# Optimization experiments

Measured on AMD Instinct MI355X. Metric: run time of the kernel, lower is better.

Reference implementation:

```python
import jax, jax.numpy as jnp
import numpy as np

B, S, D_MODEL, D_QK, D_VO = 4, 2048, 1024, 128, 128
NEG = -1.0e9


def setup_inputs() -> dict:
    key = jax.random.key(0)
    k1, k2, k3, k4, k5 = jax.random.split(key, 5)
    enc = jax.random.normal(k1, (B, S, D_MODEL), dtype=jnp.float32)
    # causal mask: True means masked (masked_fill), broadcast over batch
    causal = jnp.triu(jnp.ones((S, S), dtype=bool), k=1)
    mask = jnp.broadcast_to(causal, (B, S, S))
    scale = 0.02
    W_q = jax.random.normal(k2, (D_MODEL, D_QK), dtype=jnp.float32) * scale
    W_k = jax.random.normal(k3, (D_MODEL, D_QK), dtype=jnp.float32) * scale
    W_v = jax.random.normal(k4, (D_MODEL, D_VO), dtype=jnp.float32) * scale
    W_o = jax.random.normal(k5, (D_VO, D_MODEL), dtype=jnp.float32) * scale
    return {"encodings": enc, "mask": mask, "W_q": W_q, "W_k": W_k, "W_v": W_v, "W_o": W_o}


def reference(encodings, mask, W_q, W_k, W_v, W_o):
    # q,k: [B,S,d_qk]; v: [B,S,d_vo]
    q = jnp.einsum('bsd,de->bse', encodings, W_q)
    k = jnp.einsum('bsd,de->bse', encodings, W_k)
    v = jnp.einsum('bsd,de->bse', encodings, W_v)
    sims = jnp.einsum('bqe,bke->bqk', q, k) / jnp.asarray(D_QK ** 0.5, q.dtype)
    sims = jnp.where(mask, jnp.asarray(NEG, sims.dtype), sims)
    attn = jax.nn.softmax(sims, axis=-1)  # [B,S,S]
    scores = jnp.einsum('bqk,bke->bqe', attn, v)  # [B,S,d_vo]
    return jnp.einsum('bse,ed->bsd', scores, W_o)  # [B,S,d_model]
```

## Files before the change

### kernel.cpp

```cpp
#include <hip/hip_runtime.h>
#include <hip/hip_bf16.h>
#include <stdint.h>

typedef __attribute__((ext_vector_type(8))) short short8;
typedef __attribute__((ext_vector_type(4))) float floatx4;

using bf16 = __hip_bfloat16;

#define SCALE_L2 0.12751793359133147f

__device__ inline unsigned short f2b(float f) {
    bf16 h = __float2bfloat16(f);
    return *(unsigned short*)&h;
}
__device__ inline float b2f(unsigned short u) {
    union { unsigned int i; float f; } v;
    v.i = ((unsigned int)u) << 16;
    return v.f;
}

__device__ __forceinline__ void gll16(const bf16* g, bf16* l) {
    __builtin_amdgcn_global_load_lds((__attribute__((address_space(1))) void*)g,
                                     (__attribute__((address_space(3))) void*)l,
                                     16, 0, 0);
}

__global__ __launch_bounds__(256) void prep_w(const float* __restrict__ Wq,
                                              const float* __restrict__ Wk,
                                              const float* __restrict__ Wv,
                                              const float* __restrict__ Wo,
                                              bf16* __restrict__ Wqkvt,
                                              bf16* __restrict__ Wot) {
    int idx = blockIdx.x * 256 + threadIdx.x;
    int sel = idx >> 17;
    int i = idx & 131071;
    if (sel < 3) {
        const float* W = (sel == 0) ? Wq : (sel == 1) ? Wk : Wv;
        int r = i >> 7, c = i & 127;
        Wqkvt[(size_t)(sel * 128 + c) * 1024 + r] = __float2bfloat16(W[i]);
    } else {
        int r = i >> 10, c = i & 1023;
        Wot[(size_t)c * 128 + r] = __float2bfloat16(Wo[i]);
    }
}

__global__ __launch_bounds__(256) void gemm_qkv(const float* __restrict__ enc,
                                                const bf16* __restrict__ Bt,
                                                bf16* __restrict__ Qb,
                                                bf16* __restrict__ Kb,
                                                bf16* __restrict__ Vtb) {
    __shared__ __align__(16) bf16 As[64 * 32];
    __shared__ __align__(16) bf16 Bs[64 * 32];

    const int tid = threadIdx.x;
    const int m0 = blockIdx.x * 64;
    const int by = blockIdx.y;
    const int nsel = by >> 1;
    const int nh = by & 1;
    const int brow0 = nsel * 128 + nh * 64;
    const int w = tid >> 6, lane = tid & 63;
    const int wm = (w >> 1) * 32, wn = (w & 1) * 32;
    const int quad = lane >> 4, l16 = lane & 15;

    const int ar = tid >> 2, akq = (tid & 3) * 8;
    bf16* Bs_w = &Bs[w * 512];

    const float4* Arow = (const float4*)&enc[(size_t)(m0 + ar) * 1024];
    const int af = (tid & 3) * 2;
    float4 a0 = Arow[af], a1 = Arow[af + 1];

    floatx4 acc[2][2];
#pragma unroll
    for (int i = 0; i < 2; i++)
#pragma unroll
        for (int j = 0; j < 2; j++) acc[i][j] = (floatx4){0.f, 0.f, 0.f, 0.f};

    for (int k0 = 0; k0 < 1024; k0 += 32) {
        __syncthreads();
        gll16(&Bt[(size_t)(brow0 + ar) * 1024 + k0 + akq], Bs_w);
        ushort4 u0, u1;
        u0.x = f2b(a0.x); u0.y = f2b(a0.y); u0.z = f2b(a0.z); u0.w = f2b(a0.w);
        u1.x = f2b(a1.x); u1.y = f2b(a1.y); u1.z = f2b(a1.z); u1.w = f2b(a1.w);
        *(ushort4*)&As[ar * 32 + akq] = u0;
        *(ushort4*)&As[ar * 32 + akq + 4] = u1;
        __syncthreads();

        if (k0 + 32 < 1024) {
            a0 = Arow[((k0 + 32) >> 2) + af];
            a1 = Arow[((k0 + 32) >> 2) + af + 1];
        }

        short8 a[2], bfr[2];
#pragma unroll
        for (int mt = 0; mt < 2; mt++)
            a[mt] = *(const short8*)&As[(wm + mt * 16 + l16) * 32 + quad * 8];
#pragma unroll
        for (int nt = 0; nt < 2; nt++)
            bfr[nt] = *(const short8*)&Bs[(wn + nt * 16 + l16) * 32 + quad * 8];
#pragma unroll
        for (int mt = 0; mt < 2; mt++)
#pragma unroll
            for (int nt = 0; nt < 2; nt++)
                acc[mt][nt] = __builtin_amdgcn_mfma_f32_16x16x32_bf16(a[mt], bfr[nt], acc[mt][nt], 0, 0, 0);
    }

#pragma unroll
    for (int mt = 0; mt < 2; mt++)
#pragma unroll
        for (int nt = 0; nt < 2; nt++)
#pragma unroll
            for (int r = 0; r < 4; r++) {
                int row = m0 + wm + mt * 16 + quad * 4 + r;
                int col = nh * 64 + wn + nt * 16 + l16;
                bf16 h = __float2bfloat16(acc[mt][nt][r]);
                if (nsel == 0) {
                    Qb[(size_t)row * 128 + col] = h;
                } else if (nsel == 1) {
                    Kb[(size_t)row * 128 + col] = h;
                } else {
                    int bb = row >> 11, ss = row & 2047;
                    Vtb[(size_t)bb * 262144 + (size_t)col * 2048 + ss] = h;
                }
            }
}

__global__ __launch_bounds__(256) void gemm_out(const bf16* __restrict__ A,
                                                const bf16* __restrict__ Bt,
                                                float* __restrict__ C) {
    __shared__ bf16 As[64 * 40];
    __shared__ bf16 Bs[128 * 40];

    const int tid = threadIdx.x;
    const int m0 = blockIdx.x * 64;
    const int n0 = blockIdx.y * 128;
    const int w = tid >> 6, lane = tid & 63;
    const int wm = (w >> 1) * 32, wn = (w & 1) * 64;
    const int quad = lane >> 4, l16 = lane & 15;

    const int ra = tid >> 2, ca = (tid & 3) * 8;
    const int rb0 = tid >> 2, rb1 = (tid + 256) >> 2;

    floatx4 acc[2][4];
#pragma unroll
    for (int i = 0; i < 2; i++)
#pragma unroll
        for (int j = 0; j < 4; j++) acc[i][j] = (floatx4){0.f, 0.f, 0.f, 0.f};

    int4 pa  = *(const int4*)&A[(size_t)(m0 + ra) * 128 + ca];
    int4 pb0 = *(const int4*)&Bt[(size_t)(n0 + rb0) * 128 + ca];
    int4 pb1 = *(const int4*)&Bt[(size_t)(n0 + rb1) * 128 + ca];

    for (int k0 = 0; k0 < 128; k0 += 32) {
        __syncthreads();
        *(int4*)&As[ra * 40 + ca] = pa;
        *(int4*)&Bs[rb0 * 40 + ca] = pb0;
        *(int4*)&Bs[rb1 * 40 + ca] = pb1;
        __syncthreads();

        if (k0 + 32 < 128) {
            pa  = *(const int4*)&A[(size_t)(m0 + ra) * 128 + k0 + 32 + ca];
            pb0 = *(const int4*)&Bt[(size_t)(n0 + rb0) * 128 + k0 + 32 + ca];
            pb1 = *(const int4*)&Bt[(size_t)(n0 + rb1) * 128 + k0 + 32 + ca];
        }

        short8 a[2], b[4];
#pragma unroll
        for (int mt = 0; mt < 2; mt++)
            a[mt] = *(const short8*)&As[(wm + mt * 16 + l16) * 40 + quad * 8];
#pragma unroll
        for (int nt = 0; nt < 4; nt++)
            b[nt] = *(const short8*)&Bs[(wn + nt * 16 + l16) * 40 + quad * 8];
#pragma unroll
        for (int mt = 0; mt < 2; mt++)
#pragma unroll
            for (int nt = 0; nt < 4; nt++)
                acc[mt][nt] = __builtin_amdgcn_mfma_f32_16x16x32_bf16(a[mt], b[nt], acc[mt][nt], 0, 0, 0);
    }

#pragma unroll
    for (int mt = 0; mt < 2; mt++)
#pragma unroll
        for (int nt = 0; nt < 4; nt++)
#pragma unroll
            for (int r = 0; r < 4; r++) {
                int row = m0 + wm + mt * 16 + quad * 4 + r;
                int col = n0 + wn + nt * 16 + l16;
                C[(size_t)row * 1024 + col] = acc[mt][nt][r];
            }
}

__global__ __launch_bounds__(256) void flash_split(const bf16* __restrict__ Q,
                                                   const bf16* __restrict__ K,
                                                   const bf16* __restrict__ Vt,
                                                   bf16* __restrict__ Opb,
                                                   float2* __restrict__ Ml) {
    __shared__ __align__(16) bf16 Ks[64 * 128];
    __shared__ __align__(16) bf16 Vs[128 * 64];
    __shared__ __align__(16) bf16 Pw[4 * 2176];

    const int tid = threadIdx.x;
    const int x = blockIdx.x;
    const int b = x / 272;
    const int id = x - b * 272;
    int qt = (int)__builtin_amdgcn_sqrtf(4.0f * (float)id + 1.0f) - 1;
    if (qt < 0) qt = 0;
    while (((qt + 2) * (qt + 2)) / 4 <= id) qt++;
    while (((qt + 1) * (qt + 1)) / 4 > id) qt--;
    const int c = id - ((qt + 1) * (qt + 1)) / 4;
    const int q0 = qt * 64;
    const int start = 2 * c;
    const int end = min(start + 2, qt + 1);

    const int w = tid >> 6, lane = tid & 63;
    const int quad = lane >> 4, l16 = lane & 15;
    bf16* myP = &Pw[w * 2176];

    const int krow = w * 4 + (lane >> 4);
    const int kcb  = (lane & 15) * 16;
    const int vrow = w * 8 + (lane >> 3);
    const int vcb  = (lane & 7) * 16;
    const int ksw  = (l16 & 7) << 4;

    const int qrow = q0 + w * 16 + l16;
    const bf16* Qrow = &Q[((size_t)b * 2048 + qrow) * 128];
    short8 qf[4];
#pragma unroll
    for (int k4 = 0; k4 < 4; k4++)
        qf[k4] = *(const short8*)&Qrow[k4 * 32 + quad * 8];

    float m_run = -1.0e30f, l_run = 0.f;
    floatx4 o[8];
#pragma unroll
    for (int d = 0; d < 8; d++) o[d] = (floatx4){0.f, 0.f, 0.f, 0.f};

    {
        const int kt = start;
#pragma unroll
        for (int i = 0; i < 4; i++) {
            int row = i * 16 + krow;
            int cbs = kcb ^ ((row & 7) << 4);
            gll16(&K[((size_t)b * 2048 + kt * 64 + row) * 128 + (cbs >> 1)],
                  &Ks[i * 2048 + w * 512]);
        }
#pragma unroll
        for (int i = 0; i < 4; i++) {
            int row = i * 32 + vrow;
            int cbs = vcb ^ ((row & 7) << 4);
            gll16(&Vt[(size_t)b * 262144 + (size_t)row * 2048 + kt * 64 + (cbs >> 1)],
                  &Vs[i * 2048 + w * 512]);
        }
    }
    __syncthreads();

    for (int kt = start; kt < end; kt++) {
        floatx4 s_acc[4];
#pragma unroll
        for (int nt = 0; nt < 4; nt++) {
            s_acc[nt] = (floatx4){0.f, 0.f, 0.f, 0.f};
#pragma unroll
            for (int k4 = 0; k4 < 4; k4++) {
                short8 kf = *(const short8*)((const char*)Ks +
                              (nt * 16 + l16) * 256 + ((k4 * 64 + quad * 16) ^ ksw));
                s_acc[nt] = __builtin_amdgcn_mfma_f32_16x16x32_bf16(kf, qf[k4], s_acc[nt], 0, 0, 0);
            }
        }

        float sv[4][4];
#pragma unroll
        for (int nt = 0; nt < 4; nt++)
#pragma unroll
            for (int r = 0; r < 4; r++) {
                float s = s_acc[nt][r] * SCALE_L2;
                if (kt == qt) {
                    int kcol = kt * 64 + nt * 16 + quad * 4 + r;
                    if (kcol > qrow) s = -1.0e9f;
                }
                sv[nt][r] = s;
            }

        float t0 = fmaxf(fmaxf(sv[0][0], sv[0][1]), fmaxf(sv[0][2], sv[0][3]));
        float t1 = fmaxf(fmaxf(sv[1][0], sv[1][1]), fmaxf(sv[1][2], sv[1][3]));
        float t2 = fmaxf(fmaxf(sv[2][0], sv[2][1]), fmaxf(sv[2][2], sv[2][3]));
        float t3 = fmaxf(fmaxf(sv[3][0], sv[3][1]), fmaxf(sv[3][2], sv[3][3]));
        float tmax = fmaxf(fmaxf(t0, t1), fmaxf(t2, t3));
        tmax = fmaxf(tmax, __shfl_xor(tmax, 16));
        tmax = fmaxf(tmax, __shfl_xor(tmax, 32));

        float mnew = fmaxf(m_run, tmax);
        float alpha = exp2f(m_run - mnew);
        m_run = mnew;

        float rsum = 0.f;
#pragma unroll
        for (int nt = 0; nt < 4; nt++)
#pragma unroll
            for (int r = 0; r < 4; r++) {
                float p = exp2f(sv[nt][r] - mnew);
                sv[nt][r] = p;
                rsum += p;
            }
        rsum += __shfl_xor(rsum, 16);
        rsum += __shfl_xor(rsum, 32);
        l_run = l_run * alpha + rsum;

#pragma unroll
        for (int nt = 0; nt < 4; nt++) {
            ushort4 pk;
            pk.x = f2b(sv[nt][0]); pk.y = f2b(sv[nt][1]);
            pk.z = f2b(sv[nt][2]); pk.w = f2b(sv[nt][3]);
            *(ushort4*)&myP[l16 * 72 + nt * 16 + quad * 4] = pk;
        }

#pragma unroll
        for (int d = 0; d < 8; d++) {
            o[d][0] *= alpha; o[d][1] *= alpha; o[d][2] *= alpha; o[d][3] *= alpha;
        }

        short8 pf[2];
#pragma unroll
        for (int k2 = 0; k2 < 2; k2++)
            pf[k2] = *(const short8*)&myP[l16 * 72 + k2 * 32 + quad * 8];
#pragma unroll
        for (int d = 0; d < 8; d++)
#pragma unroll
            for (int k2 = 0; k2 < 2; k2++) {
                short8 vf = *(const short8*)((const char*)Vs +
                              (d * 16 + l16) * 128 + ((k2 * 64 + quad * 16) ^ ksw));
                o[d] = __builtin_amdgcn_mfma_f32_16x16x32_bf16(vf, pf[k2], o[d], 0, 0, 0);
            }

        if (kt + 1 < end) {
            __syncthreads();
            const int nk = kt + 1;
#pragma unroll
            for (int i = 0; i < 4; i++) {
                int row = i * 16 + krow;
                int cbs = kcb ^ ((row & 7) << 4);
                gll16(&K[((size_t)b * 2048 + nk * 64 + row) * 128 + (cbs >> 1)],
                      &Ks[i * 2048 + w * 512]);
            }
#pragma unroll
            for (int i = 0; i < 4; i++) {
                int row = i * 32 + vrow;
                int cbs = vcb ^ ((row & 7) << 4);
                gll16(&Vt[(size_t)b * 262144 + (size_t)row * 2048 + nk * 64 + (cbs >> 1)],
                      &Vs[i * 2048 + w * 512]);
            }
            __syncthreads();
        }
    }

#pragma unroll
    for (int d = 0; d < 8; d++) {
        ushort4 pk;
        pk.x = f2b(o[d][0]); pk.y = f2b(o[d][1]);
        pk.z = f2b(o[d][2]); pk.w = f2b(o[d][3]);
        *(ushort4*)&myP[l16 * 136 + d * 16 + quad * 4] = pk;
    }
    const int er = lane >> 2;
    const int ec = lane & 3;
    const size_t orow = ((size_t)x * 64 + w * 16 + er) * 128;
#pragma unroll
    for (int p = 0; p < 4; p++) {
        int ce = (p * 4 + ec) * 8;
        short8 t = *(const short8*)&myP[er * 136 + ce];
        *(short8*)&Opb[orow + ce] = t;
    }
    if (lane < 16) Ml[(size_t)x * 64 + w * 16 + l16] = make_float2(m_run, l_run);
}

__global__ __launch_bounds__(256) void flash_merge(const bf16* __restrict__ Opb,
                                                   const float2* __restrict__ Ml,
                                                   bf16* __restrict__ Sc) {
    int idx = blockIdx.x * 256 + threadIdx.x;
    int row = idx >> 5, dg = (idx & 31) * 4;
    int b = row >> 11, s = row & 2047;
    int qt = s >> 6, rl = s & 63;
    int nc = (qt >> 1) + 1;
    int id0 = b * 272 + ((qt + 1) * (qt + 1)) / 4;

    float M = -1.0e30f;
    for (int j = 0; j < nc; j++)
        M = fmaxf(M, Ml[(size_t)(id0 + j) * 64 + rl].x);

    float L = 0.f;
    float a0 = 0.f, a1 = 0.f, a2 = 0.f, a3 = 0.f;
    for (int j = 0; j < nc; j++) {
        float2 t = Ml[(size_t)(id0 + j) * 64 + rl];
        float wj = exp2f(t.x - M);
        L += t.y * wj;
        ushort4 p = *(const ushort4*)&Opb[((size_t)(id0 + j) * 64 + rl) * 128 + dg];
        a0 += wj * b2f(p.x); a1 += wj * b2f(p.y);
        a2 += wj * b2f(p.z); a3 += wj * b2f(p.w);
    }
    float inv = 1.0f / L;
    ushort4 o;
    o.x = f2b(a0 * inv); o.y = f2b(a1 * inv);
    o.z = f2b(a2 * inv); o.w = f2b(a3 * inv);
    *(ushort4*)&Sc[(size_t)row * 128 + dg] = o;
}

extern "C" void kernel_launch(void* const* d_in, const int* in_sizes, int n_in,
                              void* d_out, int out_size, void* d_ws, size_t ws_size,
                              hipStream_t stream) {
    const float* enc = (const float*)d_in[0];
    const float* Wq = (const float*)d_in[2];
    const float* Wk = (const float*)d_in[3];
    const float* Wv = (const float*)d_in[4];
    const float* Wo = (const float*)d_in[5];
    float* out = (float*)d_out;

    const size_t MB = 1024 * 1024;
    char* ws = (char*)d_ws;
    bf16*   Qb    = (bf16*)(ws);
    bf16*   Kb    = (bf16*)(ws + 2 * MB);
    bf16*   Vtb   = (bf16*)(ws + 4 * MB);
    bf16*   Scb   = (bf16*)(ws + 6 * MB);
    bf16*   Wqkvt = (bf16*)(ws + 8 * MB);
    bf16*   Wot   = (bf16*)(ws + 8 * MB + 768 * 1024);
    float2* Ml    = (float2*)(ws + 9 * MB);
    bf16*   Opb   = (bf16*)(ws + 10 * MB);

    prep_w<<<2048, dim3(256), 0, stream>>>(Wq, Wk, Wv, Wo, Wqkvt, Wot);

    gemm_qkv<<<dim3(128, 6), dim3(256), 0, stream>>>(enc, Wqkvt, Qb, Kb, Vtb);

    flash_split<<<1088, dim3(256), 0, stream>>>(Qb, Kb, Vtb, Opb, Ml);
    flash_merge<<<1024, dim3(256), 0, stream>>>(Opb, Ml, Scb);

    gemm_out<<<dim3(128, 8), dim3(256), 0, stream>>>(Scb, Wot, out);
}
```

Baseline: 188.8 us.

## Preload both KV tiles in flash_split and reshape QKV GEMM tiles

The flash_split kernel now loads both of its K/V tiles (at most two per block) into separate shared-memory buffers up front, which removes the mid-loop barrier pair and the serialized second load. Shared memory grows to about 73KB per block, which may reduce blocks per CU. The P scratch buffer is shrunk, and the output staging reuses the K/V region after a final barrier. Separately, gemm_qkv switches from 64x64 tiles to 32x128 tiles, so each block covers a full Q, K or V output width and the encodings are converted to bf16 once per 128 columns instead of twice.

```diff
diff --git a/kernel.cpp b/kernel.cpp
--- a/kernel.cpp
+++ b/kernel.cpp
@@ -49,79 +49,65 @@
                                                 bf16* __restrict__ Qb,
                                                 bf16* __restrict__ Kb,
                                                 bf16* __restrict__ Vtb) {
-    __shared__ __align__(16) bf16 As[64 * 32];
-    __shared__ __align__(16) bf16 Bs[64 * 32];
+    __shared__ __align__(16) bf16 As[32 * 32];
+    __shared__ __align__(16) bf16 Bs[128 * 32];
 
     const int tid = threadIdx.x;
-    const int m0 = blockIdx.x * 64;
-    const int by = blockIdx.y;
-    const int nsel = by >> 1;
-    const int nh = by & 1;
-    const int brow0 = nsel * 128 + nh * 64;
+    const int m0 = blockIdx.x * 32;
+    const int nsel = blockIdx.y;
+    const int brow0 = nsel * 128;
     const int w = tid >> 6, lane = tid & 63;
-    const int wm = (w >> 1) * 32, wn = (w & 1) * 32;
+    const int wr = (w >> 1) * 16, wc = (w & 1) * 64;
     const int quad = lane >> 4, l16 = lane & 15;
 
-    const int ar = tid >> 2, akq = (tid & 3) * 8;
-    bf16* Bs_w = &Bs[w * 512];
-
-    const float4* Arow = (const float4*)&enc[(size_t)(m0 + ar) * 1024];
-    const int af = (tid & 3) * 2;
-    float4 a0 = Arow[af], a1 = Arow[af + 1];
-
-    floatx4 acc[2][2];
-#pragma unroll
-    for (int i = 0; i < 2; i++)
-#pragma unroll
-        for (int j = 0; j < 2; j++) acc[i][j] = (floatx4){0.f, 0.f, 0.f, 0.f};
+    const int ar = tid >> 3, af = tid & 7;
+    const int br = w * 16 + (lane >> 2), bk = (lane & 3) * 8;
+
+    const float4* Arow4 = (const float4*)&enc[(size_t)(m0 + ar) * 1024];
+    float4 a0 = Arow4[af];
+
+    floatx4 acc[4];
+#pragma unroll
+    for (int j = 0; j < 4; j++) acc[j] = (floatx4){0.f, 0.f, 0.f, 0.f};
 
     for (int k0 = 0; k0 < 1024; k0 += 32) {
         __syncthreads();
-        gll16(&Bt[(size_t)(brow0 + ar) * 1024 + k0 + akq], Bs_w);
-        ushort4 u0, u1;
+        gll16(&Bt[(size_t)(brow0 + br) * 1024 + k0 + bk], &Bs[w * 512]);
+        gll16(&Bt[(size_t)(brow0 + 64 + br) * 1024 + k0 + bk], &Bs[2048 + w * 512]);
+        ushort4 u0;
         u0.x = f2b(a0.x); u0.y = f2b(a0.y); u0.z = f2b(a0.z); u0.w = f2b(a0.w);
-        u1.x = f2b(a1.x); u1.y = f2b(a1.y); u1.z = f2b(a1.z); u1.w = f2b(a1.w);
-        *(ushort4*)&As[ar * 32 + akq] = u0;
-        *(ushort4*)&As[ar * 32 + akq + 4] = u1;
+        *(ushort4*)&As[ar * 32 + af * 4] = u0;
         __syncthreads();
 
-        if (k0 + 32 < 1024) {
-            a0 = Arow[((k0 + 32) >> 2) + af];
-            a1 = Arow[((k0 + 32) >> 2) + af + 1];
-        }
-
-        short8 a[2], bfr[2];
-#pragma unroll
-        for (int mt = 0; mt < 2; mt++)
-            a[mt] = *(const short8*)&As[(wm + mt * 16 + l16) * 32 + quad * 8];
-#pragma unroll
-        for (int nt = 0; nt < 2; nt++)
-            bfr[nt] = *(const short8*)&Bs[(wn + nt * 16 + l16) * 32 + quad * 8];
-#pragma unroll
-        for (int mt = 0; mt < 2; mt++)
-#pragma unroll
-            for (int nt = 0; nt < 2; nt++)
-                acc[mt][nt] = __builtin_amdgcn_mfma_f32_16x16x32_bf16(a[mt], bfr[nt], acc[mt][nt], 0, 0, 0);
-    }
-
-#pragma unroll
-    for (int mt = 0; mt < 2; mt++)
-#pragma unroll
-        for (int nt = 0; nt < 2; nt++)
-#pragma unroll
-            for (int r = 0; r < 4; r++) {
-                int row = m0 + wm + mt * 16 + quad * 4 + r;
-                int col = nh * 64 + wn + nt * 16 + l16;
-                bf16 h = __float2bfloat16(acc[mt][nt][r]);
-                if (nsel == 0) {
-                    Qb[(size_t)row * 128 + col] = h;
-                } else if (nsel == 1) {
-                    Kb[(size_t)row * 128 + col] = h;
-                } else {
-                    int bb = row >> 11, ss = row & 2047;
-                    Vtb[(size_t)bb * 262144 + (size_t)col * 2048 + ss] = h;
-                }
-            }
+        if (k0 + 32 < 1024)
+            a0 = Arow4[((k0 + 32) >> 2) + af];
+
+        short8 a = *(const short8*)&As[(wr + l16) * 32 + quad * 8];
+        short8 bfr[4];
+#pragma unroll
+        for (int nt = 0; nt < 4; nt++)
+            bfr[nt] = *(const short8*)&Bs[(wc + nt * 16 + l16) * 32 + quad * 8];
+#pragma unroll
+        for (int nt = 0; nt < 4; nt++)
+            acc[nt] = __builtin_amdgcn_mfma_f32_16x16x32_bf16(a, bfr[nt], acc[nt], 0, 0, 0);
+    }
+
+#pragma unroll
+    for (int nt = 0; nt < 4; nt++)
+#pragma unroll
+        for (int r = 0; r < 4; r++) {
+            int row = m0 + wr + quad * 4 + r;
+            int col = wc + nt * 16 + l16;
+            bf16 h = __float2bfloat16(acc[nt][r]);
+            if (nsel == 0) {
+                Qb[(size_t)row * 128 + col] = h;
+            } else if (nsel == 1) {
+                Kb[(size_t)row * 128 + col] = h;
+            } else {
+                int bb = row >> 11, ss = row & 2047;
+                Vtb[(size_t)bb * 262144 + (size_t)col * 2048 + ss] = h;
+            }
+        }
 }
 
 __global__ __launch_bounds__(256) void gemm_out(const bf16* __restrict__ A,
@@ -194,9 +180,7 @@
                                                    const bf16* __restrict__ Vt,
                                                    bf16* __restrict__ Opb,
                                                    float2* __restrict__ Ml) {
-    __shared__ __align__(16) bf16 Ks[64 * 128];
-    __shared__ __align__(16) bf16 Vs[128 * 64];
-    __shared__ __align__(16) bf16 Pw[4 * 2176];
+    __shared__ __align__(16) char smem[74752];
 
     const int tid = threadIdx.x;
     const int x = blockIdx.x;
@@ -213,7 +197,7 @@
 
     const int w = tid >> 6, lane = tid & 63;
     const int quad = lane >> 4, l16 = lane & 15;
-    bf16* myP = &Pw[w * 2176];
+    bf16* myP = (bf16*)(smem + 65536) + w * 1152;
 
     const int krow = w * 4 + (lane >> 4);
     const int kcb  = (lane & 15) * 16;
@@ -233,33 +217,39 @@
 #pragma unroll
     for (int d = 0; d < 8; d++) o[d] = (floatx4){0.f, 0.f, 0.f, 0.f};
 
-    {
-        const int kt = start;
+#pragma unroll 1
+    for (int t = 0; t < 2; t++) {
+        if (start + t >= end) break;
+        const int kt = start + t;
+        char* base = smem + t * 32768;
 #pragma unroll
         for (int i = 0; i < 4; i++) {
             int row = i * 16 + krow;
             int cbs = kcb ^ ((row & 7) << 4);
             gll16(&K[((size_t)b * 2048 + kt * 64 + row) * 128 + (cbs >> 1)],
-                  &Ks[i * 2048 + w * 512]);
+                  (bf16*)(base + i * 4096 + w * 1024));
         }
 #pragma unroll
         for (int i = 0; i < 4; i++) {
             int row = i * 32 + vrow;
             int cbs = vcb ^ ((row & 7) << 4);
             gll16(&Vt[(size_t)b * 262144 + (size_t)row * 2048 + kt * 64 + (cbs >> 1)],
-                  &Vs[i * 2048 + w * 512]);
+                  (bf16*)(base + 16384 + i * 4096 + w * 1024));
         }
     }
     __syncthreads();
 
     for (int kt = start; kt < end; kt++) {
+        const char* Kb = smem + ((kt - start) & 1) * 32768;
+        const char* Vb = Kb + 16384;
+
         floatx4 s_acc[4];
 #pragma unroll
         for (int nt = 0; nt < 4; nt++) {
             s_acc[nt] = (floatx4){0.f, 0.f, 0.f, 0.f};
 #pragma unroll
             for (int k4 = 0; k4 < 4; k4++) {
-                short8 kf = *(const short8*)((const char*)Ks +
+                short8 kf = *(const short8*)(Kb +
                               (nt * 16 + l16) * 256 + ((k4 * 64 + quad * 16) ^ ksw));
                 s_acc[nt] = __builtin_amdgcn_mfma_f32_16x16x32_bf16(kf, qf[k4], s_acc[nt], 0, 0, 0);
             }
@@ -324,38 +314,20 @@
         for (int d = 0; d < 8; d++)
 #pragma unroll
             for (int k2 = 0; k2 < 2; k2++) {
-                short8 vf = *(const short8*)((const char*)Vs +
+                short8 vf = *(const short8*)(Vb +
                               (d * 16 + l16) * 128 + ((k2 * 64 + quad * 16) ^ ksw));
                 o[d] = __builtin_amdgcn_mfma_f32_16x16x32_bf16(vf, pf[k2], o[d], 0, 0, 0);
             }
-
-        if (kt + 1 < end) {
-            __syncthreads();
-            const int nk = kt + 1;
-#pragma unroll
-            for (int i = 0; i < 4; i++) {
-                int row = i * 16 + krow;
-                int cbs = kcb ^ ((row & 7) << 4);
-                gll16(&K[((size_t)b * 2048 + nk * 64 + row) * 128 + (cbs >> 1)],
-                      &Ks[i * 2048 + w * 512]);
-            }
-#pragma unroll
-            for (int i = 0; i < 4; i++) {
-                int row = i * 32 + vrow;
-                int cbs = vcb ^ ((row & 7) << 4);
-                gll16(&Vt[(size_t)b * 262144 + (size_t)row * 2048 + nk * 64 + (cbs >> 1)],
-                      &Vs[i * 2048 + w * 512]);
-            }
-            __syncthreads();
-        }
-    }
-
+    }
+
+    __syncthreads();
+    bf16* myO = (bf16*)(smem + w * 4352);
 #pragma unroll
     for (int d = 0; d < 8; d++) {
         ushort4 pk;
         pk.x = f2b(o[d][0]); pk.y = f2b(o[d][1]);
         pk.z = f2b(o[d][2]); pk.w = f2b(o[d][3]);
-        *(ushort4*)&myP[l16 * 136 + d * 16 + quad * 4] = pk;
+        *(ushort4*)&myO[l16 * 136 + d * 16 + quad * 4] = pk;
     }
     const int er = lane >> 2;
     const int ec = lane & 3;
@@ -363,7 +335,7 @@
 #pragma unroll
     for (int p = 0; p < 4; p++) {
         int ce = (p * 4 + ec) * 8;
-        short8 t = *(const short8*)&myP[er * 136 + ce];
+        short8 t = *(const short8*)&myO[er * 136 + ce];
         *(short8*)&Opb[orow + ce] = t;
     }
     if (lane < 16) Ml[(size_t)x * 64 + w * 16 + l16] = make_float2(m_run, l_run);
@@ -423,7 +395,7 @@
 
     prep_w<<<2048, dim3(256), 0, stream>>>(Wq, Wk, Wv, Wo, Wqkvt, Wot);
 
-    gemm_qkv<<<dim3(128, 6), dim3(256), 0, stream>>>(enc, Wqkvt, Qb, Kb, Vtb);
+    gemm_qkv<<<dim3(256, 3), dim3(256), 0, stream>>>(enc, Wqkvt, Qb, Kb, Vtb);
 
     flash_split<<<1088, dim3(256), 0, stream>>>(Qb, Kb, Vtb, Opb, Ml);
     flash_merge<<<1024, dim3(256), 0, stream>>>(Opb, Ml, Scb);
```

Result: no change. 190.0 us (+0.6%).
